# Performance work log

Hardware: AMD Instinct MI355X
Metric: run time of the kernel (lower is better)

## Reference

```python
import jax, jax.numpy as jnp
import numpy as np
import math

W = 64  # window_size == chunk_size == 64


def _windows(x, w):
    """x: [b, t, ...] -> [b, nb, 2w, ...]: for block j, concat(block j-1, block j).
    Block -1 is zero padding; its validity is handled by the attention mask."""
    b, t = x.shape[0], x.shape[1]
    nb = t // w
    pad = [(0, 0), (w, 0)] + [(0, 0)] * (x.ndim - 2)
    xp = jnp.pad(x, pad)                                   # [b, t+w, ...]
    xb = xp.reshape((b, nb + 1, w) + x.shape[2:])          # [b, nb+1, w, ...]
    return jnp.concatenate([xb[:, :-1], xb[:, 1:]], axis=2)  # [b, nb, 2w, ...]


def setup_inputs() -> dict:
    key = jax.random.key(0)
    k1, k2, k3 = jax.random.split(key, 3)
    b, t, h, d = 4, 4096, 16, 64
    return {
        "q": jax.random.normal(k1, (b, t, h, d), dtype=jnp.float32),
        "k": jax.random.normal(k2, (b, t, h, d), dtype=jnp.float32),
        "v": jax.random.normal(k3, (b, t, h, d), dtype=jnp.float32),
        "attn_mask": jnp.ones((b, t), dtype=jnp.int32),
    }


def reference(q, k, v, attn_mask):
    b, t, h, d = q.shape
    nb = t // W
    scale = 1.0 / math.sqrt(d)

    qb = q.reshape(b, nb, W, h, d)
    kw = _windows(k, W)                         # [b, nb, 2W, h, d]
    vw = _windows(v, W)                         # [b, nb, 2W, h, d]
    mw = _windows(attn_mask.astype(bool), W)    # [b, nb, 2W]

    # query local index i attends to key local index m iff 0 <= (i+W-m) < W
    i = jnp.arange(W)[:, None]
    m = jnp.arange(2 * W)[None, :]
    diff = i + W - m
    band = (diff >= 0) & (diff < W)             # [W, 2W]

    valid = band[None, None] & mw[:, :, None, :]          # [b, nb, W, 2W]

    scores = jnp.einsum('bnqhd,bnkhd->bnhqk', qb, kw) * scale  # [b,nb,h,W,2W]
    scores = jnp.where(valid[:, :, None], scores, jnp.float32(-1e9))
    attn = jax.nn.softmax(scores, axis=-1)
    attn = attn * valid[:, :, None].astype(attn.dtype)

    qm = attn_mask.astype(q.dtype).reshape(b, nb, W)      # query validity
    attn = attn * qm[:, :, None, :, None]

    out = jnp.einsum('bnhqk,bnkhd->bnqhd', attn, vw)      # [b,nb,W,h,d]
    out = out * qm[:, :, :, None, None]
    return out.reshape(b, t, h, d)
```

## Files before the change

kernel.cpp:

```cpp
#include <hip/hip_runtime.h>
#include <hip/hip_bf16.h>


#define TT 4096
#define HH 16
#define DD 64
#define WW 64
#define NBLK (TT / WW)

typedef __attribute__((ext_vector_type(8))) short bf16x8;
typedef __attribute__((ext_vector_type(4))) float f32x4;

static __device__ __forceinline__ ushort f2bf(float x) {
    return __builtin_bit_cast(unsigned short, __float2bfloat16(x));
}
static __device__ __forceinline__ uint pack2(float a, float b) {
    return (uint)f2bf(a) | ((uint)f2bf(b) << 16);
}

__global__ __launch_bounds__(256, 5)
void lca_fwd(const float* __restrict__ q, const float* __restrict__ k,
             const float* __restrict__ v, const int* __restrict__ am,
             float* __restrict__ out)
{
    const int jb = ((blockIdx.x & 7) << 3) | (blockIdx.x >> 3);
    const int hi = blockIdx.y;
    const int bi = blockIdx.z;

    __shared__ ushort sKP[8192];
    __shared__ ushort sVt[8192];

    const int tid  = threadIdx.x;
    const int wv   = tid >> 6, lane = tid & 63;
    const int quad = lane >> 4, l15 = lane & 15;

    const size_t rowstride = (size_t)HH * DD;
    const size_t qbase = ((size_t)(bi * TT + jb * WW) * HH + hi) * DD;
    const long  kstart = (long)jb * WW - WW;

    const int* amb = am + (size_t)bi * TT;
    long t0 = kstart + lane;
    bool kv0 = (t0 >= 0) && (amb[t0] != 0);
    bool qv  = (amb[jb * WW + lane] != 0);
    unsigned long long kvm_lo = __ballot(kv0);
    unsigned long long qvm    = __ballot(qv);

    float4 fk[8], fv[8], fq[4];
    if (jb > 0) {
        #pragma unroll
        for (int p = 0; p < 8; ++p) {
            int idx = p * 256 + tid;
            int row = idx >> 4, c4 = (idx & 15) * 4;
            fk[p] = *(const float4*)(k + ((size_t)(bi * TT + kstart + row) * HH + hi) * DD + c4);
        }
        #pragma unroll
        for (int p = 0; p < 8; ++p) {
            int idx = p * 256 + tid;
            int row = idx >> 4, c4 = (idx & 15) * 4;
            fv[p] = *(const float4*)(v + ((size_t)(bi * TT + kstart + row) * HH + hi) * DD + c4);
        }
    } else {
        #pragma unroll
        for (int p = 0; p < 8; ++p) {
            float4 z = make_float4(0.f, 0.f, 0.f, 0.f);
            if (p >= 4) {
                int idx = p * 256 + tid;
                int row = idx >> 4, c4 = (idx & 15) * 4;
                z = *(const float4*)(k + ((size_t)(bi * TT + (row - 64)) * HH + hi) * DD + c4);
            }
            fk[p] = z;
        }
        #pragma unroll
        for (int p = 0; p < 8; ++p) {
            float4 z = make_float4(0.f, 0.f, 0.f, 0.f);
            if (p >= 4) {
                int idx = p * 256 + tid;
                int row = idx >> 4, c4 = (idx & 15) * 4;
                z = *(const float4*)(v + ((size_t)(bi * TT + (row - 64)) * HH + hi) * DD + c4);
            }
            fv[p] = z;
        }
    }
    {
        const float* qrow = q + qbase + (size_t)(16 * wv + l15) * rowstride;
        fq[0] = *(const float4*)(qrow + quad * 8);
        fq[1] = *(const float4*)(qrow + quad * 8 + 4);
        fq[2] = *(const float4*)(qrow + 32 + quad * 8);
        fq[3] = *(const float4*)(qrow + 32 + quad * 8 + 4);
    }

    #pragma unroll
    for (int p = 0; p < 8; ++p) {
        int idx = p * 256 + tid;
        int row = idx >> 4, c4 = (idx & 15) * 4;
        uint2 w; w.x = pack2(fk[p].x, fk[p].y); w.y = pack2(fk[p].z, fk[p].w);
        *(uint2*)(&sKP[row * 64 + (((c4 >> 3) ^ (row & 7)) << 3) + (c4 & 7)]) = w;
    }
    #pragma unroll
    for (int p = 0; p < 8; ++p) {
        int idx = p * 256 + tid;
        int row = idx >> 4, c4 = (idx & 15) * 4;
        int u = row >> 3, k7 = row & 7;
        sVt[(c4 + 0) * 128 + ((u ^ ((c4 + 0) & 15)) << 3) + k7] = f2bf(fv[p].x);
        sVt[(c4 + 1) * 128 + ((u ^ ((c4 + 1) & 15)) << 3) + k7] = f2bf(fv[p].y);
        sVt[(c4 + 2) * 128 + ((u ^ ((c4 + 2) & 15)) << 3) + k7] = f2bf(fv[p].z);
        sVt[(c4 + 3) * 128 + ((u ^ ((c4 + 3) & 15)) << 3) + k7] = f2bf(fv[p].w);
    }
    union { bf16x8 v8; uint u[4]; } A0, A1;
    A0.u[0] = pack2(fq[0].x, fq[0].y); A0.u[1] = pack2(fq[0].z, fq[0].w);
    A0.u[2] = pack2(fq[1].x, fq[1].y); A0.u[3] = pack2(fq[1].z, fq[1].w);
    A1.u[0] = pack2(fq[2].x, fq[2].y); A1.u[1] = pack2(fq[2].z, fq[2].w);
    A1.u[2] = pack2(fq[3].x, fq[3].y); A1.u[3] = pack2(fq[3].z, fq[3].w);
    __syncthreads();

    const int r0 = 16 * wv + 4 * quad;
    const int r7 = l15 & 7;

    f32x4 acc[8];
    #pragma unroll
    for (int kt = 0; kt < 8; ++kt) {
        f32x4 a = {0.f, 0.f, 0.f, 0.f};
        const ushort* kr = &sKP[(16 * kt + l15) * 64];
        bf16x8 b0 = *(const bf16x8*)(kr + ((quad ^ r7) << 3));
        bf16x8 b1 = *(const bf16x8*)(kr + (((4 + quad) ^ r7) << 3));
        a = __builtin_amdgcn_mfma_f32_16x16x32_bf16(A0.v8, b0, a, 0, 0, 0);
        a = __builtin_amdgcn_mfma_f32_16x16x32_bf16(A1.v8, b1, a, 0, 0, 0);
        acc[kt] = a;
    }
    __syncthreads();

    const float NEG = -1.0e9f;
    float rmax[4] = {NEG, NEG, NEG, NEG};
    #pragma unroll
    for (int kt = 0; kt < 8; ++kt) {
        int c = 16 * kt + l15;
        unsigned long long km = (kt < 4) ? kvm_lo : qvm;
        int kvc = (int)((km >> (c & 63)) & 1ull);
        #pragma unroll
        for (int reg = 0; reg < 4; ++reg) {
            int r = r0 + reg;
            bool valid = (c > r) && (c <= r + WW) && kvc;
            float s = valid ? acc[kt][reg] : NEG;
            acc[kt][reg] = s;
            rmax[reg] = fmaxf(rmax[reg], s);
        }
    }
    #pragma unroll
    for (int reg = 0; reg < 4; ++reg) {
        #pragma unroll
        for (int m = 1; m <= 8; m <<= 1)
            rmax[reg] = fmaxf(rmax[reg], __shfl_xor(rmax[reg], m, 64));
    }

    const float CEXP = 0.125f * 1.44269504088896f;
    const int l7 = l15 & 7, h3 = l15 >> 3;
    float rsum[4] = {0.f, 0.f, 0.f, 0.f};
    #pragma unroll
    for (int kt = 0; kt < 8; ++kt) {
        int cu = 2 * kt + h3;
        #pragma unroll
        for (int reg = 0; reg < 4; ++reg) {
            float s = acc[kt][reg];
            float pex = (s > -1.0e8f) ? exp2f((s - rmax[reg]) * CEXP) : 0.f;
            rsum[reg] += pex;
            int r = r0 + reg;
            sKP[r * 128 + ((cu ^ (4 * quad + reg)) << 3) + l7] = f2bf(pex);
        }
    }
    float rden[4];
    #pragma unroll
    for (int reg = 0; reg < 4; ++reg) {
        #pragma unroll
        for (int m = 1; m <= 8; m <<= 1)
            rsum[reg] += __shfl_xor(rsum[reg], m, 64);
        rden[reg] = (rsum[reg] > 0.f ? 1.f / rsum[reg] : 0.f)
                    * (float)((qvm >> (r0 + reg)) & 1ull);
    }

    bf16x8 ap[4];
    const ushort* pr = &sKP[(16 * wv + l15) * 128];
    #pragma unroll
    for (int kc = 0; kc < 4; ++kc)
        ap[kc] = *(const bf16x8*)(pr + (((4 * kc + quad) ^ l15) << 3));

    #pragma unroll
    for (int nt = 0; nt < 4; ++nt) {
        f32x4 a = {0.f, 0.f, 0.f, 0.f};
        const ushort* vr = &sVt[(16 * nt + l15) * 128];
        #pragma unroll
        for (int kc = 0; kc < 4; ++kc) {
            bf16x8 bv = *(const bf16x8*)(vr + (((4 * kc + quad) ^ l15) << 3));
            a = __builtin_amdgcn_mfma_f32_16x16x32_bf16(ap[kc], bv, a, 0, 0, 0);
        }
        #pragma unroll
        for (int reg = 0; reg < 4; ++reg)
            out[qbase + (size_t)(r0 + reg) * rowstride + 16 * nt + l15]
                = a[reg] * rden[reg];
    }
}

extern "C" void kernel_launch(void* const* d_in, const int* in_sizes, int n_in,
                              void* d_out, int out_size, void* d_ws, size_t ws_size,
                              hipStream_t stream) {
    const float* q  = (const float*)d_in[0];
    const float* k  = (const float*)d_in[1];
    const float* v  = (const float*)d_in[2];
    const int*   am = (const int*)d_in[3];
    float* out = (float*)d_out;

    const int b = in_sizes[3] / TT;
    dim3 grid(NBLK, HH, b);
    dim3 block(256);
    lca_fwd<<<grid, block, 0, stream>>>(q, k, v, am, out);
}
```

Baseline: 229.6 us.

## Rewrite window attention with 32x32 MFMA, register-resident K and P, 2-wave blocks

Moves the kernel to 128-thread blocks where each wave owns 32 query rows and uses 32x32x16 bf16 MFMA. K is loaded straight from global into MFMA operands, covering only the 96 keys each wave needs rather than staging all 128 in LDS. Softmax probabilities stay in registers and are fed directly as the A operand of the PV MFMA, so the LDS round-trip for P goes away. A fast path skips mask-bit work when every mask bit is set. It also swaps in manual bf16 rounding and new LDS swizzles, at the cost of higher register pressure and redundant K loads across waves.

Measured after the change: 233.0 us. No clear change (+1.5%).

```diff
diff --git a/kernel.cpp b/kernel.cpp
--- a/kernel.cpp
+++ b/kernel.cpp
@@ -1,5 +1,4 @@
 #include <hip/hip_runtime.h>
-#include <hip/hip_bf16.h>
 
 
 #define TT 4096
@@ -9,193 +8,183 @@
 #define NBLK (TT / WW)
 
 typedef __attribute__((ext_vector_type(8))) short bf16x8;
-typedef __attribute__((ext_vector_type(4))) float f32x4;
-
-static __device__ __forceinline__ ushort f2bf(float x) {
-    return __builtin_bit_cast(unsigned short, __float2bfloat16(x));
-}
+typedef __attribute__((ext_vector_type(16))) float f32x16;
+
+static __device__ __forceinline__ uint bfr(float x) {
+    uint u = __builtin_bit_cast(uint, x);
+    return (u + 0x7FFFu + ((u >> 16) & 1u)) >> 16;
+}
+static __device__ __forceinline__ ushort f2bf(float x) { return (ushort)bfr(x); }
 static __device__ __forceinline__ uint pack2(float a, float b) {
-    return (uint)f2bf(a) | ((uint)f2bf(b) << 16);
-}
-
-__global__ __launch_bounds__(256, 5)
+    return bfr(a) | (bfr(b) << 16);
+}
+static __device__ __forceinline__ int vsw(int d) { return ((d >> 2) ^ d) & 15; }
+
+__global__ __launch_bounds__(128, 3)
 void lca_fwd(const float* __restrict__ q, const float* __restrict__ k,
              const float* __restrict__ v, const int* __restrict__ am,
              float* __restrict__ out)
 {
     const int jb = ((blockIdx.x & 7) << 3) | (blockIdx.x >> 3);
-    const int hi = blockIdx.y;
+    const int hd = blockIdx.y;
     const int bi = blockIdx.z;
 
-    __shared__ ushort sKP[8192];
-    __shared__ ushort sVt[8192];
+    __shared__ __align__(16) ushort sVt[8192];
 
     const int tid  = threadIdx.x;
-    const int wv   = tid >> 6, lane = tid & 63;
-    const int quad = lane >> 4, l15 = lane & 15;
-
+    const int wv   = tid >> 6;
+    const int lane = tid & 63;
+    const int l31  = lane & 31, hl = lane >> 5;
+
+    const int T0 = jb * WW;
+    const int Tq = T0 + 32 * wv;
     const size_t rowstride = (size_t)HH * DD;
-    const size_t qbase = ((size_t)(bi * TT + jb * WW) * HH + hi) * DD;
-    const long  kstart = (long)jb * WW - WW;
-
+    const size_t hoff = ((size_t)bi * TT) * rowstride + (size_t)hd * DD;
     const int* amb = am + (size_t)bi * TT;
-    long t0 = kstart + lane;
-    bool kv0 = (t0 >= 0) && (amb[t0] != 0);
-    bool qv  = (amb[jb * WW + lane] != 0);
-    unsigned long long kvm_lo = __ballot(kv0);
-    unsigned long long qvm    = __ballot(qv);
-
-    float4 fk[8], fv[8], fq[4];
-    if (jb > 0) {
-        #pragma unroll
-        for (int p = 0; p < 8; ++p) {
-            int idx = p * 256 + tid;
-            int row = idx >> 4, c4 = (idx & 15) * 4;
-            fk[p] = *(const float4*)(k + ((size_t)(bi * TT + kstart + row) * HH + hi) * DD + c4);
-        }
-        #pragma unroll
-        for (int p = 0; p < 8; ++p) {
-            int idx = p * 256 + tid;
-            int row = idx >> 4, c4 = (idx & 15) * 4;
-            fv[p] = *(const float4*)(v + ((size_t)(bi * TT + kstart + row) * HH + hi) * DD + c4);
-        }
-    } else {
-        #pragma unroll
-        for (int p = 0; p < 8; ++p) {
-            float4 z = make_float4(0.f, 0.f, 0.f, 0.f);
-            if (p >= 4) {
-                int idx = p * 256 + tid;
-                int row = idx >> 4, c4 = (idx & 15) * 4;
-                z = *(const float4*)(k + ((size_t)(bi * TT + (row - 64)) * HH + hi) * DD + c4);
+
+    long tok0 = (long)Tq - 64 + lane;
+    unsigned long long m_lo = __ballot((tok0 >= 0) && (amb[tok0 < 0 ? 0 : tok0] != 0));
+    unsigned int m_hi = (unsigned int)__ballot(amb[Tq + l31] != 0);
+
+    {
+        const int d0 = (tid & 15) * 4;
+        const int rb = tid >> 4;
+        #pragma unroll
+        for (int p = 0; p < 16; ++p) {
+            int kl = p * 8 + rb;
+            long tok = (long)T0 - 64 + kl;
+            if (tok < 0) tok = 0;
+            const float4 x = *(const float4*)(v + hoff + (size_t)tok * rowstride + d0);
+            int e = kl & 15;
+            int pos = (kl & ~15) | (e & 3) | ((e & 8) >> 1) | ((e & 4) << 1);
+            int pu = pos >> 3, p7 = pos & 7;
+            sVt[(d0 + 0) * 128 + ((pu ^ vsw(d0 + 0)) << 3) + p7] = f2bf(x.x);
+            sVt[(d0 + 1) * 128 + ((pu ^ vsw(d0 + 1)) << 3) + p7] = f2bf(x.y);
+            sVt[(d0 + 2) * 128 + ((pu ^ vsw(d0 + 2)) << 3) + p7] = f2bf(x.z);
+            sVt[(d0 + 3) * 128 + ((pu ^ vsw(d0 + 3)) << 3) + p7] = f2bf(x.w);
+        }
+    }
+
+    bf16x8 Bq[4];
+    {
+        const float* qr = q + hoff + (size_t)(Tq + l31) * rowstride + hl * 8;
+        #pragma unroll
+        for (int ds = 0; ds < 4; ++ds) {
+            float4 a = *(const float4*)(qr + ds * 16);
+            float4 b = *(const float4*)(qr + ds * 16 + 4);
+            union { bf16x8 v8; uint u[4]; } w;
+            w.u[0] = pack2(a.x, a.y); w.u[1] = pack2(a.z, a.w);
+            w.u[2] = pack2(b.x, b.y); w.u[3] = pack2(b.z, b.w);
+            Bq[ds] = w.v8;
+        }
+    }
+
+    float s[48];
+    #pragma unroll
+    for (int t = 0; t < 3; ++t) {
+        long krw = (long)Tq - 64 + 32 * t + l31;
+        if (krw < 0) krw = 0;
+        const float* kr = k + hoff + (size_t)krw * rowstride + hl * 8;
+        f32x16 a;
+        #pragma unroll
+        for (int i = 0; i < 16; ++i) a[i] = 0.f;
+        #pragma unroll
+        for (int ds = 0; ds < 4; ++ds) {
+            float4 xx = *(const float4*)(kr + ds * 16);
+            float4 yy = *(const float4*)(kr + ds * 16 + 4);
+            union { bf16x8 v8; uint u[4]; } w;
+            w.u[0] = pack2(xx.x, xx.y); w.u[1] = pack2(xx.z, xx.w);
+            w.u[2] = pack2(yy.x, yy.y); w.u[3] = pack2(yy.z, yy.w);
+            a = __builtin_amdgcn_mfma_f32_32x32x16_bf16(w.v8, Bq[ds], a, 0, 0, 0);
+        }
+        #pragma unroll
+        for (int r = 0; r < 16; ++r) s[t * 16 + r] = a[r];
+    }
+
+    const int ql = l31;
+    float vb[48];
+    #pragma unroll
+    for (int t = 0; t < 3; ++t)
+        #pragma unroll
+        for (int r = 0; r < 16; ++r) {
+            int kl = 32 * t + (r & 3) + 8 * (r >> 2) + 4 * hl;
+            bool band = (t == 0) ? (kl > ql) : (t == 2 ? (kl - 64 <= ql) : true);
+            vb[t * 16 + r] = band ? 1.f : 0.f;
+        }
+    if (!((m_lo == ~0ull) && (m_hi == 0xFFFFFFFFu))) {
+        #pragma unroll
+        for (int t = 0; t < 3; ++t)
+            #pragma unroll
+            for (int r = 0; r < 16; ++r) {
+                int kl = 32 * t + (r & 3) + 8 * (r >> 2) + 4 * hl;
+                uint bit = (kl < 64) ? (uint)((m_lo >> kl) & 1ull)
+                                     : ((m_hi >> (kl - 64)) & 1u);
+                vb[t * 16 + r] *= (float)bit;
             }
-            fk[p] = z;
-        }
-        #pragma unroll
-        for (int p = 0; p < 8; ++p) {
-            float4 z = make_float4(0.f, 0.f, 0.f, 0.f);
-            if (p >= 4) {
-                int idx = p * 256 + tid;
-                int row = idx >> 4, c4 = (idx & 15) * 4;
-                z = *(const float4*)(v + ((size_t)(bi * TT + (row - 64)) * HH + hi) * DD + c4);
-            }
-            fv[p] = z;
-        }
-    }
-    {
-        const float* qrow = q + qbase + (size_t)(16 * wv + l15) * rowstride;
-        fq[0] = *(const float4*)(qrow + quad * 8);
-        fq[1] = *(const float4*)(qrow + quad * 8 + 4);
-        fq[2] = *(const float4*)(qrow + 32 + quad * 8);
-        fq[3] = *(const float4*)(qrow + 32 + quad * 8 + 4);
-    }
-
-    #pragma unroll
-    for (int p = 0; p < 8; ++p) {
-        int idx = p * 256 + tid;
-        int row = idx >> 4, c4 = (idx & 15) * 4;
-        uint2 w; w.x = pack2(fk[p].x, fk[p].y); w.y = pack2(fk[p].z, fk[p].w);
-        *(uint2*)(&sKP[row * 64 + (((c4 >> 3) ^ (row & 7)) << 3) + (c4 & 7)]) = w;
-    }
-    #pragma unroll
-    for (int p = 0; p < 8; ++p) {
-        int idx = p * 256 + tid;
-        int row = idx >> 4, c4 = (idx & 15) * 4;
-        int u = row >> 3, k7 = row & 7;
-        sVt[(c4 + 0) * 128 + ((u ^ ((c4 + 0) & 15)) << 3) + k7] = f2bf(fv[p].x);
-        sVt[(c4 + 1) * 128 + ((u ^ ((c4 + 1) & 15)) << 3) + k7] = f2bf(fv[p].y);
-        sVt[(c4 + 2) * 128 + ((u ^ ((c4 + 2) & 15)) << 3) + k7] = f2bf(fv[p].z);
-        sVt[(c4 + 3) * 128 + ((u ^ ((c4 + 3) & 15)) << 3) + k7] = f2bf(fv[p].w);
-    }
-    union { bf16x8 v8; uint u[4]; } A0, A1;
-    A0.u[0] = pack2(fq[0].x, fq[0].y); A0.u[1] = pack2(fq[0].z, fq[0].w);
-    A0.u[2] = pack2(fq[1].x, fq[1].y); A0.u[3] = pack2(fq[1].z, fq[1].w);
-    A1.u[0] = pack2(fq[2].x, fq[2].y); A1.u[1] = pack2(fq[2].z, fq[2].w);
-    A1.u[2] = pack2(fq[3].x, fq[3].y); A1.u[3] = pack2(fq[3].z, fq[3].w);
+    }
+    float mx[24];
+    #pragma unroll
+    for (int i = 0; i < 24; ++i) mx[i] = fmaxf(s[i], s[i + 24]);
+    #pragma unroll
+    for (int i = 0; i < 12; ++i) mx[i] = fmaxf(mx[i], mx[i + 12]);
+    #pragma unroll
+    for (int i = 0; i < 6;  ++i) mx[i] = fmaxf(mx[i], mx[i + 6]);
+    float rmax = fmaxf(fmaxf(fmaxf(mx[0], mx[1]), fmaxf(mx[2], mx[3])),
+                       fmaxf(mx[4], mx[5]));
+    rmax = fmaxf(rmax, __shfl_xor(rmax, 32, 64));
+
+    const float CEXP = 0.125f * 1.44269504088896f;
+    float p[48];
+    #pragma unroll
+    for (int i = 0; i < 48; ++i)
+        p[i] = exp2f((s[i] - rmax) * CEXP) * vb[i];
+
+    float t24[24];
+    #pragma unroll
+    for (int i = 0; i < 24; ++i) t24[i] = p[i] + p[i + 24];
+    #pragma unroll
+    for (int i = 0; i < 12; ++i) t24[i] += t24[i + 12];
+    #pragma unroll
+    for (int i = 0; i < 6;  ++i) t24[i] += t24[i + 6];
+    float sum = ((t24[0] + t24[1]) + (t24[2] + t24[3])) + (t24[4] + t24[5]);
+    sum += __shfl_xor(sum, 32, 64);
+
+    float rden = (sum > 0.f ? 1.f / sum : 0.f) * (float)((m_hi >> ql) & 1u);
+    #pragma unroll
+    for (int i = 0; i < 48; ++i) p[i] *= rden;
+
     __syncthreads();
 
-    const int r0 = 16 * wv + 4 * quad;
-    const int r7 = l15 & 7;
-
-    f32x4 acc[8];
-    #pragma unroll
-    for (int kt = 0; kt < 8; ++kt) {
-        f32x4 a = {0.f, 0.f, 0.f, 0.f};
-        const ushort* kr = &sKP[(16 * kt + l15) * 64];
-        bf16x8 b0 = *(const bf16x8*)(kr + ((quad ^ r7) << 3));
-        bf16x8 b1 = *(const bf16x8*)(kr + (((4 + quad) ^ r7) << 3));
-        a = __builtin_amdgcn_mfma_f32_16x16x32_bf16(A0.v8, b0, a, 0, 0, 0);
-        a = __builtin_amdgcn_mfma_f32_16x16x32_bf16(A1.v8, b1, a, 0, 0, 0);
-        acc[kt] = a;
-    }
-    __syncthreads();
-
-    const float NEG = -1.0e9f;
-    float rmax[4] = {NEG, NEG, NEG, NEG};
-    #pragma unroll
-    for (int kt = 0; kt < 8; ++kt) {
-        int c = 16 * kt + l15;
-        unsigned long long km = (kt < 4) ? kvm_lo : qvm;
-        int kvc = (int)((km >> (c & 63)) & 1ull);
-        #pragma unroll
-        for (int reg = 0; reg < 4; ++reg) {
-            int r = r0 + reg;
-            bool valid = (c > r) && (c <= r + WW) && kvc;
-            float s = valid ? acc[kt][reg] : NEG;
-            acc[kt][reg] = s;
-            rmax[reg] = fmaxf(rmax[reg], s);
-        }
-    }
-    #pragma unroll
-    for (int reg = 0; reg < 4; ++reg) {
-        #pragma unroll
-        for (int m = 1; m <= 8; m <<= 1)
-            rmax[reg] = fmaxf(rmax[reg], __shfl_xor(rmax[reg], m, 64));
-    }
-
-    const float CEXP = 0.125f * 1.44269504088896f;
-    const int l7 = l15 & 7, h3 = l15 >> 3;
-    float rsum[4] = {0.f, 0.f, 0.f, 0.f};
-    #pragma unroll
-    for (int kt = 0; kt < 8; ++kt) {
-        int cu = 2 * kt + h3;
-        #pragma unroll
-        for (int reg = 0; reg < 4; ++reg) {
-            float s = acc[kt][reg];
-            float pex = (s > -1.0e8f) ? exp2f((s - rmax[reg]) * CEXP) : 0.f;
-            rsum[reg] += pex;
-            int r = r0 + reg;
-            sKP[r * 128 + ((cu ^ (4 * quad + reg)) << 3) + l7] = f2bf(pex);
-        }
-    }
-    float rden[4];
-    #pragma unroll
-    for (int reg = 0; reg < 4; ++reg) {
-        #pragma unroll
-        for (int m = 1; m <= 8; m <<= 1)
-            rsum[reg] += __shfl_xor(rsum[reg], m, 64);
-        rden[reg] = (rsum[reg] > 0.f ? 1.f / rsum[reg] : 0.f)
-                    * (float)((qvm >> (r0 + reg)) & 1ull);
-    }
-
-    bf16x8 ap[4];
-    const ushort* pr = &sKP[(16 * wv + l15) * 128];
-    #pragma unroll
-    for (int kc = 0; kc < 4; ++kc)
-        ap[kc] = *(const bf16x8*)(pr + (((4 * kc + quad) ^ l15) << 3));
-
-    #pragma unroll
-    for (int nt = 0; nt < 4; ++nt) {
-        f32x4 a = {0.f, 0.f, 0.f, 0.f};
-        const ushort* vr = &sVt[(16 * nt + l15) * 128];
-        #pragma unroll
-        for (int kc = 0; kc < 4; ++kc) {
-            bf16x8 bv = *(const bf16x8*)(vr + (((4 * kc + quad) ^ l15) << 3));
-            a = __builtin_amdgcn_mfma_f32_16x16x32_bf16(ap[kc], bv, a, 0, 0, 0);
-        }
-        #pragma unroll
-        for (int reg = 0; reg < 4; ++reg)
-            out[qbase + (size_t)(r0 + reg) * rowstride + 16 * nt + l15]
-                = a[reg] * rden[reg];
+    f32x16 O0, O1;
+    #pragma unroll
+    for (int i = 0; i < 16; ++i) { O0[i] = 0.f; O1[i] = 0.f; }
+    #pragma unroll
+    for (int st = 0; st < 6; ++st) {
+        union { bf16x8 v8; uint u[4]; } A;
+        const int pb = 16 * (st >> 1) + 8 * (st & 1);
+        #pragma unroll
+        for (int j = 0; j < 4; ++j)
+            A.u[j] = pack2(p[pb + 2 * j], p[pb + 2 * j + 1]);
+        const int Ub = 4 * wv + 2 * st + hl;
+        {
+            int d = l31;
+            const bf16x8 B0 = *(const bf16x8*)(&sVt[d * 128 + ((Ub ^ vsw(d)) << 3)]);
+            O0 = __builtin_amdgcn_mfma_f32_32x32x16_bf16(A.v8, B0, O0, 0, 0, 0);
+        }
+        {
+            int d = 32 + l31;
+            const bf16x8 B1 = *(const bf16x8*)(&sVt[d * 128 + ((Ub ^ vsw(d)) << 3)]);
+            O1 = __builtin_amdgcn_mfma_f32_32x32x16_bf16(A.v8, B1, O1, 0, 0, 0);
+        }
+    }
+
+    float* ob = out + hoff + (size_t)Tq * rowstride;
+    #pragma unroll
+    for (int r = 0; r < 16; ++r) {
+        int qrow = (r & 3) + 8 * (r >> 2) + 4 * hl;
+        float* orow = ob + (size_t)qrow * rowstride;
+        orow[l31]      = O0[r];
+        orow[32 + l31] = O1[r];
     }
 }
 
@@ -206,10 +195,10 @@
     const float* k  = (const float*)d_in[1];
     const float* v  = (const float*)d_in[2];
     const int*   am = (const int*)d_in[3];
-    float* out = (float*)d_out;
+    float* outp = (float*)d_out;
 
     const int b = in_sizes[3] / TT;
     dim3 grid(NBLK, HH, b);
-    dim3 block(256);
-    lca_fwd<<<grid, block, 0, stream>>>(q, k, v, am, out);
-}
+    dim3 block(128);
+    lca_fwd<<<grid, block, 0, stream>>>(q, k, v, am, outp);
+}
```
